# Kernel optimization log

Hardware: AMD Instinct MI355X
Metric: run time of the kernel (lower is better)

The kernel has to match this reference:

```python
import jax
import jax.numpy as jnp
import numpy as np
from jax.scipy.linalg import expm

H = 2048   # hidden_size
R = 1      # low-rank dimension
B = 2048   # batch of independent (h, x) pairs


def _glorot(key, shape):
    return jax.random.uniform(key, shape, minval=-1.0, maxval=1.0) * jnp.sqrt(2.0 / sum(shape))


def setup_inputs() -> dict:
    key = jax.random.key(0)
    k1, k2, k3, k4, k5, k6 = jax.random.split(key, 6)
    return {
        "h": jax.random.normal(k5, (B, H), dtype=jnp.float32),
        "x": jax.random.normal(k6, (B, H), dtype=jnp.float32),
        # a_diag ~ U(-1, 0) * init_scale (10.0): negative real diagonal
        "a_diag": jax.random.uniform(k1, (H,), minval=-1.0, maxval=0.0) * 10.0,
        "p_vec": _glorot(k2, (H, R)),
        "q_vec": _glorot(k3, (H, R)),
        "b_mat": _glorot(k4, (H, H)),
        "delta": jnp.array(0.1, dtype=jnp.float32),
    }


def reference(h, x, a_diag, p_vec, q_vec, b_mat, delta):
    # A = diag(a_diag) + P Q^T  (DPLR structure, materialized dense as in source)
    A = jnp.diag(a_diag) + p_vec @ q_vec.T                       # [H, H]
    # Discretized state matrix: exp(delta * A)
    expA = expm(delta * A)                                       # [H, H]
    # Discretized input matrix: A^{-1} (exp(delta A) - I) B  (pinv as in source)
    A_inv = jnp.linalg.pinv(A)                                   # [H, H]
    B_disc = A_inv @ (expA - jnp.eye(H, dtype=A.dtype)) @ b_mat  # [H, H]
    # Batched recurrence step: A h + B x  for each row of h, x
    return h @ expA.T + x @ B_disc.T                             # [B, H]
```

## Files before the change

kernel.cpp:

```cpp
#include <hip/hip_runtime.h>

#define MAXM 16
#define NL_CAP 256
#define THETA 0.02f
#define SMEM_BYTES 32768

typedef unsigned short u16;
typedef u16 u16x8 __attribute__((ext_vector_type(8)));
typedef u16 u16x4 __attribute__((ext_vector_type(4)));
typedef __bf16 bf16x8 __attribute__((ext_vector_type(8)));
typedef float f32x4 __attribute__((ext_vector_type(4)));


__device__ __forceinline__ u16 f2bf(float f) {
    unsigned u = __float_as_uint(f);
    return (u16)((u + 0x7fffu + ((u >> 16) & 1u)) >> 16);
}

__global__ __launch_bounds__(256)
void conv_k(const float* __restrict__ x, const float* __restrict__ b,
            u16* __restrict__ xb, u16* __restrict__ bb, long nx, long nb)
{
    long i = ((long)blockIdx.x * 256 + threadIdx.x) * 4;
    if (i < nx) {
        float4 v = *(const float4*)&x[i];
        u16x4 o = {f2bf(v.x), f2bf(v.y), f2bf(v.z), f2bf(v.w)};
        *(u16x4*)&xb[i] = o;
    }
    if (i < nb) {
        float4 v = *(const float4*)&b[i];
        u16x4 o = {f2bf(v.x), f2bf(v.y), f2bf(v.z), f2bf(v.w)};
        *(u16x4*)&bb[i] = o;
    }
}


__device__ __forceinline__ double frcp(double den) {
    double r = (double)__builtin_amdgcn_rcpf((float)den);
    return fma(r, fma(-den, r, 1.0), r);
}


__device__ __forceinline__ void gload_lds16(const void* g, void* l) {
    __builtin_amdgcn_global_load_lds(
        (const __attribute__((address_space(1))) unsigned int*)g,
        (__attribute__((address_space(3))) unsigned int*)l, 16, 0, 0);
}

__device__ __forceinline__ void gemm_tile(u16* Al, u16* Bl, int tid, int bx, int by,
                                          const u16* __restrict__ A,
                                          const u16* __restrict__ B,
                                          float* __restrict__ C,
                                          int Ndim, int Kstride, int Klen)
{
    const int bm = by * 128, bn = bx * 128;
    const int wv = tid >> 6, ln = tid & 63;
    const int wr = (wv >> 1) * 64, wc = (wv & 1) * 64;
    const int fr = ln & 15, fk = (ln >> 4) * 8;
    const int fk2 = fk ^ ((fr & 3) << 3);

    const int r0 = tid >> 2;
    const int c0 = ((tid & 3) ^ (r0 & 3)) * 8;
    const u16* Ap0 = A + (size_t)(bm + r0) * Kstride + c0;
    const u16* Ap1 = Ap0 + (size_t)64 * Kstride;
    const u16* Bp0 = B + (size_t)(bn + r0) * Kstride + c0;
    const u16* Bp1 = Bp0 + (size_t)64 * Kstride;

    f32x4 acc[4][4];
#pragma unroll
    for (int m = 0; m < 4; ++m)
#pragma unroll
        for (int n = 0; n < 4; ++n) acc[m][n] = (f32x4)0.f;

    {
        u16* a0 = Al + wv * 512;
        u16* a1 = Al + 2048 + wv * 512;
        u16* b0 = Bl + wv * 512;
        u16* b1 = Bl + 2048 + wv * 512;
        gload_lds16(Ap0, a0);
        gload_lds16(Ap1, a1);
        gload_lds16(Bp0, b0);
        gload_lds16(Bp1, b1);
    }

    int cur = 0;
    for (int kk = 0; kk < Klen; kk += 32) {
        const bool hasNext = (kk + 32 < Klen);
        if (hasNext) {
            const int nb = (cur ^ 1) * 4096;
            u16* a0 = Al + nb + wv * 512;
            u16* a1 = Al + nb + 2048 + wv * 512;
            u16* b0 = Bl + nb + wv * 512;
            u16* b1 = Bl + nb + 2048 + wv * 512;
            gload_lds16(Ap0 + kk + 32, a0);
            gload_lds16(Ap1 + kk + 32, a1);
            gload_lds16(Bp0 + kk + 32, b0);
            gload_lds16(Bp1 + kk + 32, b1);
            asm volatile("s_waitcnt vmcnt(4)" ::: "memory");
        } else {
            asm volatile("s_waitcnt vmcnt(0)" ::: "memory");
        }
        __builtin_amdgcn_sched_barrier(0);
        __builtin_amdgcn_s_barrier();

        const int cb = cur * 4096;
        u16x8 af[4], bf[4];
#pragma unroll
        for (int m = 0; m < 4; ++m)
            af[m] = *(const u16x8*)&Al[cb + (wr + m * 16 + fr) * 32 + fk2];
#pragma unroll
        for (int n = 0; n < 4; ++n)
            bf[n] = *(const u16x8*)&Bl[cb + (wc + n * 16 + fr) * 32 + fk2];
#pragma unroll
        for (int m = 0; m < 4; ++m)
#pragma unroll
            for (int n = 0; n < 4; ++n)
                acc[m][n] = __builtin_amdgcn_mfma_f32_16x16x32_bf16(
                    __builtin_bit_cast(bf16x8, af[m]),
                    __builtin_bit_cast(bf16x8, bf[n]), acc[m][n], 0, 0, 0);

        __builtin_amdgcn_sched_barrier(0);
        __builtin_amdgcn_s_barrier();
        cur ^= 1;
    }

    const int crow = (ln >> 4) * 4;
#pragma unroll
    for (int m = 0; m < 4; ++m)
#pragma unroll
        for (int n = 0; n < 4; ++n) {
            const size_t base = (size_t)(bm + wr + m * 16 + crow) * Ndim
                              + bn + wc + n * 16 + fr;
#pragma unroll
            for (int j = 0; j < 4; ++j)
                C[base + (size_t)j * Ndim] = acc[m][n][j];
        }
}

__global__ __launch_bounds__(256)
void bgemm_k(const u16* __restrict__ A, const u16* __restrict__ B,
             float* __restrict__ C, int Ndim, int Kdim)
{
    __shared__ __align__(16) unsigned char smem[SMEM_BYTES];
    gemm_tile((u16*)smem, (u16*)smem + 8192, threadIdx.x,
              blockIdx.x, blockIdx.y, A, B, C, Ndim, Kdim, Kdim);
}


__global__ __launch_bounds__(256)
void g_sgemm_k(const float* __restrict__ A, const float* __restrict__ B,
               float* __restrict__ C, int Mdim, int Ndim, int Kdim)
{
    __shared__ __align__(16) float As[16][132];
    __shared__ __align__(16) float Bs[16][68];
    const int tid = threadIdx.x;
    const int tx = tid & 15, ty = tid >> 4;
    const int bn = blockIdx.x * 64, bm = blockIdx.y * 128;
    const int lrA = tid >> 1, lcA = (tid & 1) << 3;
    const int lrB = tid >> 2, lcB = (tid & 3) << 2;
    const float* Aptr = A + (size_t)(bm + lrA) * Kdim + lcA;
    const float* Bptr = B + (size_t)(bn + lrB) * Kdim + lcB;
    float4 a0 = *(const float4*)(Aptr);
    float4 a1 = *(const float4*)(Aptr + 4);
    float4 b0 = *(const float4*)(Bptr);
    float acc[8][4];
#pragma unroll
    for (int i = 0; i < 8; ++i)
#pragma unroll
        for (int j = 0; j < 4; ++j) acc[i][j] = 0.f;
    for (int kk = 0; kk < Kdim; kk += 16) {
        __syncthreads();
        As[lcA + 0][lrA] = a0.x; As[lcA + 1][lrA] = a0.y;
        As[lcA + 2][lrA] = a0.z; As[lcA + 3][lrA] = a0.w;
        As[lcA + 4][lrA] = a1.x; As[lcA + 5][lrA] = a1.y;
        As[lcA + 6][lrA] = a1.z; As[lcA + 7][lrA] = a1.w;
        Bs[lcB + 0][lrB] = b0.x; Bs[lcB + 1][lrB] = b0.y;
        Bs[lcB + 2][lrB] = b0.z; Bs[lcB + 3][lrB] = b0.w;
        __syncthreads();
        if (kk + 16 < Kdim) {
            a0 = *(const float4*)(Aptr + kk + 16);
            a1 = *(const float4*)(Aptr + kk + 20);
            b0 = *(const float4*)(Bptr + kk + 16);
        }
#pragma unroll
        for (int k = 0; k < 16; ++k) {
            const float4 av0 = *(const float4*)&As[k][ty * 8];
            const float4 av1 = *(const float4*)&As[k][ty * 8 + 4];
            const float4 bv  = *(const float4*)&Bs[k][tx * 4];
            const float avf[8] = {av0.x, av0.y, av0.z, av0.w, av1.x, av1.y, av1.z, av1.w};
            const float bvf[4] = {bv.x, bv.y, bv.z, bv.w};
#pragma unroll
            for (int i = 0; i < 8; ++i)
#pragma unroll
                for (int j = 0; j < 4; ++j) acc[i][j] += avf[i] * bvf[j];
        }
    }
#pragma unroll
    for (int i = 0; i < 8; ++i) {
        const int r = bm + ty * 8 + i;
        float4 v = {acc[i][0], acc[i][1], acc[i][2], acc[i][3]};
        *(float4*)&C[(size_t)r * Ndim + bn + tx * 4] = v;
    }
}


__device__ __forceinline__ double wsum(double x) {
#pragma unroll
    for (int m = 32; m; m >>= 1) x += __shfl_xor(x, m, 64);
    return x;
}
__device__ __forceinline__ float wsumf(float x) {
#pragma unroll
    for (int m = 32; m; m >>= 1) x += __shfl_xor(x, m, 64);
    return x;
}

__device__ __forceinline__ int inert(double s11, double s12, double s22,
                                     double dc, double cS)
{
    double b00 = cS - s11, b01 = -1.0 - s12, b11 = -s22;
    double det = b00 * b11 - b01 * b01, tr = b00 + b11;
    int neg = (det > 0.0) ? ((tr < 0.0) ? 2 : 0) : 1;
    return (int)(dc + 0.5) + neg - 1;
}

__device__ __forceinline__ int lane_evalN32(float tf, double td, int n4,
    const float4* l0, const float4* l1, const float4* l2,
    const double* pc, bool poly, double cS,
    double& g11o, double& g12o, double& g22o)
{
    float s11 = 0.f, s12 = 0.f, s22 = 0.f, dc = 0.f;
#pragma unroll 4
    for (int i = 0; i < n4; ++i) {
        const float4 d4 = l0[i], x4 = l1[i], y4 = l2[i];
        const float dd[4] = {d4.x, d4.y, d4.z, d4.w};
        const float xx[4] = {x4.x, x4.y, x4.z, x4.w};
        const float yy[4] = {y4.x, y4.y, y4.z, y4.w};
#pragma unroll
        for (int e = 0; e < 4; ++e) {
            float den = dd[e] - tf;
            float mag = fmaxf(fabsf(den), 1e-30f);
            den = (den < 0.f) ? -mag : mag;
            const float inv = __builtin_amdgcn_rcpf(den);
            s11 = fmaf(xx[e] * xx[e], inv, s11);
            s12 = fmaf(xx[e] * yy[e], inv, s12);
            s22 = fmaf(yy[e] * yy[e], inv, s22);
            if (dd[e] < tf) dc += 1.f;
        }
    }
    double S11 = (double)s11, S12 = (double)s12, S22 = (double)s22;
    if (poly) {
        S11 += pc[0] + td * (pc[3] + td * (pc[6] + td * pc[9]));
        S12 += pc[1] + td * (pc[4] + td * (pc[7] + td * pc[10]));
        S22 += pc[2] + td * (pc[5] + td * (pc[8] + td * pc[11]));
    }
    g11o = S11; g12o = S12; g22o = S22;
    return inert(S11, S12, S22, (double)dc, cS);
}

__device__ void spec256(unsigned char* smem, int tid,
                        const float* __restrict__ av, const float* __restrict__ pv,
                        const float* __restrict__ qv, double* __restrict__ hdr,
                        float* __restrict__ V)
{
    __builtin_amdgcn_s_setprio(1);

    float* sd2 = (float*)smem;
    float* sw1 = sd2 + 2048;
    float* sw2 = sw1 + 2048;
    float* nl0 = sw2 + 2048;
    float* nl1 = nl0 + NL_CAP;
    float* nl2 = nl1 + NL_CAP;
    double* dsh = (double*)(nl2 + NL_CAP);
    int* ish = (int*)(dsh + 192);

    const int lane = tid & 63, wv = tid >> 6;
    const int j0 = tid * 8;

    float d2r[8], w1r[8], w2r[8];
    double cS = 0, n1 = 0, n2 = 0, mx = 0;
#pragma unroll
    for (int h = 0; h < 2; ++h) {
        float4 aa = *(const float4*)&av[j0 + h * 4];
        float4 pp = *(const float4*)&pv[j0 + h * 4];
        float4 qq = *(const float4*)&qv[j0 + h * 4];
        const float a4[4] = {aa.x, aa.y, aa.z, aa.w};
        const float p4[4] = {pp.x, pp.y, pp.z, pp.w};
        const float q4[4] = {qq.x, qq.y, qq.z, qq.w};
#pragma unroll
        for (int e = 0; e < 4; ++e) {
            const int ix = h * 4 + e;
            d2r[ix] = a4[e] * a4[e];
            w1r[ix] = a4[e] * p4[e];
            w2r[ix] = q4[e];
            sd2[j0 + ix] = d2r[ix]; sw1[j0 + ix] = w1r[ix]; sw2[j0 + ix] = w2r[ix];
            cS += (double)p4[e] * p4[e];
            n1 += (double)w1r[ix] * w1r[ix];
            n2 += (double)w2r[ix] * w2r[ix];
            mx = fmax(mx, (double)d2r[ix]);
        }
    }
    cS = wsum(cS); n1 = wsum(n1); n2 = wsum(n2);
#pragma unroll
    for (int m_ = 32; m_; m_ >>= 1) mx = fmax(mx, __shfl_xor(mx, m_, 64));
    __syncthreads();
    if (lane == 0) { dsh[wv] = cS; dsh[4 + wv] = n1; dsh[8 + wv] = n2; dsh[12 + wv] = mx; }
    __syncthreads();
    cS = 0; n1 = 0; n2 = 0; mx = 0;
    for (int w = 0; w < 4; ++w) {
        cS += dsh[w]; n1 += dsh[4 + w]; n2 += dsh[8 + w];
        mx = fmax(mx, dsh[12 + w]);
    }
    __syncthreads();

    const double pert = 2.0 * sqrt(n1 * n2) + cS * n2;
    double lo = fmax(0.0, mx - pert);
    double hi = mx + pert + 0.5;
    for (int r = 0; r < 3; ++r) {
        const double td = lo + (hi - lo) * (double)(wv + 1) / 5.0;
        const float tf = (float)td;
        float s11 = 0.f, s12 = 0.f, s22 = 0.f, dc = 0.f;
        for (int i4 = lane; i4 < 512; i4 += 64) {
            const float4 dd = ((const float4*)sd2)[i4];
            const float4 e1 = ((const float4*)sw1)[i4];
            const float4 e2 = ((const float4*)sw2)[i4];
            const float df[4] = {dd.x, dd.y, dd.z, dd.w};
            const float f1[4] = {e1.x, e1.y, e1.z, e1.w};
            const float f2[4] = {e2.x, e2.y, e2.z, e2.w};
#pragma unroll
            for (int e = 0; e < 4; ++e) {
                float den = df[e] - tf;
                float mag = fmaxf(fabsf(den), 1e-30f);
                den = (den < 0.f) ? -mag : mag;
                const float inv = __builtin_amdgcn_rcpf(den);
                s11 = fmaf(f1[e] * f1[e], inv, s11);
                s12 = fmaf(f1[e] * f2[e], inv, s12);
                s22 = fmaf(f2[e] * f2[e], inv, s22);
                if (df[e] < tf) dc += 1.f;
            }
        }
        s11 = wsumf(s11); s12 = wsumf(s12); s22 = wsumf(s22); dc = wsumf(dc);
        if (lane == 0)
            ish[wv] = inert((double)s11, (double)s12, (double)s22, (double)dc, cS);
        __syncthreads();
        double nlo = lo, nhi = hi;
        for (int i = 0; i < 4; ++i) {
            double ti = lo + (hi - lo) * (double)(i + 1) / 5.0;
            if (ish[i] >= 2048) { if (ti < nhi) nhi = ti; }
            else                { if (ti > nlo) nlo = ti; }
        }
        lo = nlo; hi = nhi;
        __syncthreads();
    }
    const double lmax = 0.5 * (lo + hi);
    const double rc = 10.0 * 2048.0 * 1.1920928955078125e-07;
    const double cut2 = rc * rc * lmax;

    int flags = 0, lc = 0;
#pragma unroll
    for (int e = 0; e < 8; ++e)
        if (d2r[e] < THETA) { flags |= (1 << e); ++lc; }
    int sc = lc;
#pragma unroll
    for (int off = 1; off < 64; off <<= 1) {
        int y = __shfl_up(sc, off, 64);
        if (lane >= off) sc += y;
    }
    const int wtot = __shfl(sc, 63, 64);
    const int excl = sc - lc;
    if (lane == 0) ish[4 + wv] = wtot;
    __syncthreads();
    int base = excl;
    for (int w = 0; w < wv; ++w) base += ish[4 + w];
    int cnt = 0;
    for (int w = 0; w < 4; ++w) cnt += ish[4 + w];
    {
        int pos = base;
#pragma unroll
        for (int e = 0; e < 8; ++e) {
            if (flags & (1 << e)) {
                if (pos < NL_CAP) { nl0[pos] = d2r[e]; nl1[pos] = w1r[e]; nl2[pos] = w2r[e]; }
                ++pos;
            }
        }
    }
    const int cntPad = (cnt + 7) & ~7;
    if (tid == 0) {
        for (int i = cnt; i < cntPad && i < NL_CAP; ++i) {
            nl0[i] = 1e30f; nl1[i] = 0.f; nl2[i] = 0.f;
        }
        ish[8] = cnt; ish[10] = cntPad >> 2;
    }

    float cff[12];
#pragma unroll
    for (int c = 0; c < 12; ++c) cff[c] = 0.f;
#pragma unroll
    for (int e = 0; e < 8; ++e) {
        if (d2r[e] >= THETA) {
            float id = __builtin_amdgcn_rcpf(d2r[e]);
            float b1 = w1r[e], b2 = w2r[e];
            float x11 = b1 * b1, x12 = b1 * b2, x22 = b2 * b2;
            float f = id;
            cff[0] += x11 * f; cff[1]  += x12 * f; cff[2]  += x22 * f; f *= id;
            cff[3] += x11 * f; cff[4]  += x12 * f; cff[5]  += x22 * f; f *= id;
            cff[6] += x11 * f; cff[7]  += x12 * f; cff[8]  += x22 * f; f *= id;
            cff[9] += x11 * f; cff[10] += x12 * f; cff[11] += x22 * f;
        }
    }
#pragma unroll
    for (int c = 0; c < 12; ++c) cff[c] = wsumf(cff[c]);
    if (lane == 0) {
        double* dw = &dsh[16 + wv * 12];
#pragma unroll
        for (int c = 0; c < 12; ++c) dw[c] = (double)cff[c];
    }
    __syncthreads();
    if (tid < 12) {
        double s = 0;
        for (int w = 0; w < 4; ++w) s += dsh[16 + w * 12 + tid];
        dsh[96 + tid] = s;
    }
    __syncthreads();

    cnt = ish[8];
    const bool nearOK = (cnt <= NL_CAP - 8);
    const float4* l0 = nearOK ? (const float4*)nl0 : (const float4*)sd2;
    const float4* l1 = nearOK ? (const float4*)nl1 : (const float4*)sw1;
    const float4* l2 = nearOK ? (const float4*)nl2 : (const float4*)sw2;
    const int n4 = nearOK ? ish[10] : 512;
    const bool poly = nearOK;
    const double* pcoef = &dsh[96];

    double zg1, zg2, zg3;
    if (wv == 0) {
        int N = lane_evalN32((float)cut2, cut2, n4, l0, l1, l2, pcoef, poly, cS,
                             zg1, zg2, zg3);
        if (lane == 0) ish[9] = N;
    }
    __syncthreads();
    int m = ish[9];
    if (m < 0) m = 0;
    if (m > MAXM) m = MAXM;

    for (int k = wv; k < m; k += 4) {
        double klo = 0.0, khi = cut2;
        for (int r = 0; r < 2; ++r) {
            const double w = khi - klo;
            const double td = klo + w * (double)(lane + 1) / 65.0;
            int N = lane_evalN32((float)td, td, n4, l0, l1, l2, pcoef, poly, cS,
                                 zg1, zg2, zg3);
            unsigned long long mask = __ballot(N >= k + 1);
            int j = (mask == 0ull) ? 64 : (__ffsll(mask) - 1);
            double nk = (j == 64) ? khi : (klo + w * (double)(j + 1) / 65.0);
            klo = klo + w * (double)j / 65.0;
            khi = nk;
        }
        const double lam = 0.5 * (klo + khi);
        double g11, g12, g22;
        lane_evalN32((float)lam, lam, n4, l0, l1, l2, pcoef, poly, cS, g11, g12, g22);
        const double m00 = 1.0 + g12, m01 = g11 + cS * g12;
        const double m10 = g22,       m11 = 1.0 + g12 + cS * g22;
        double y1, y2;
        if (m00 * m00 + m01 * m01 >= m10 * m10 + m11 * m11) { y1 = m01; y2 = -m00; }
        else                                                { y1 = m11; y2 = -m10; }
        double z1 = y2, z2 = y1 + cS * y2;
        const double zs = 1.0 / fmax(fmax(fabs(z1), fabs(z2)), 1e-300);
        if (lane == 0) {
            dsh[112 + 3 * k]     = lam;
            dsh[112 + 3 * k + 1] = z1 * zs;
            dsh[112 + 3 * k + 2] = z2 * zs;
        }
    }
    __syncthreads();

    for (int k = 0; k < m; ++k) {
        const double lam = dsh[112 + 3 * k];
        const float z1 = (float)dsh[112 + 3 * k + 1];
        const float z2 = (float)dsh[112 + 3 * k + 2];
        float vr[8];
        float pn = 0.f;
#pragma unroll
        for (int e = 0; e < 8; ++e) {
            const double dend = (double)d2r[e] - lam;
            float den = (float)dend;
            float mag = fmaxf(fabsf(den), 1e-12f);
            den = (den < 0.f) ? -mag : mag;
            const float vi = (w1r[e] * z1 + w2r[e] * z2) * __builtin_amdgcn_rcpf(den);
            pn = fmaf(vi, vi, pn);
            vr[e] = vi;
        }
        pn = wsumf(pn);
        if (lane == 0) dsh[160 + wv] = (double)pn;
        __syncthreads();
        double tot = 0;
        for (int w = 0; w < 4; ++w) tot += dsh[160 + w];
        const float inv = (float)(1.0 / sqrt(tot));
        float o0[8];
#pragma unroll
        for (int e = 0; e < 8; ++e) o0[e] = vr[e] * inv;
        *(float4*)&V[(size_t)k * 2048 + j0]     = *(float4*)&o0[0];
        *(float4*)&V[(size_t)k * 2048 + j0 + 4] = *(float4*)&o0[4];
        __syncthreads();
    }

    if (tid == 0) { hdr[0] = lmax; hdr[1] = cut2; hdr[2] = (double)m; hdr[3] = cS; }
    __builtin_amdgcn_s_setprio(0);
}


__global__ __launch_bounds__(256)
void fat_k(const u16* __restrict__ A, const u16* __restrict__ B,
           float* __restrict__ C0, float* __restrict__ C1,
           float* __restrict__ C2, float* __restrict__ C3,
           int Ndim, int Kdim, int ntiles, int nbx, int nsplit,
           const float* __restrict__ av, const float* __restrict__ pv,
           const float* __restrict__ qv, double* __restrict__ hdr,
           float* __restrict__ V)
{
    __shared__ __align__(16) unsigned char smem[SMEM_BYTES];
    const int bid = blockIdx.x;
    if (bid == 0) {
        spec256(smem, threadIdx.x, av, pv, qv, hdr, V);
        return;
    }
    if ((bid & 255) == 0) return;
    const int t = bid - 1 - (bid >> 8);
    if (t >= ntiles * nsplit) return;
    const int ks = t / ntiles;
    const int tt = t - ks * ntiles;
    const int Klen = Kdim / nsplit;
    float* Cdst = (ks == 0) ? C0 : (ks == 1) ? C1 : (ks == 2) ? C2 : C3;
    gemm_tile((u16*)smem, (u16*)smem + 8192, threadIdx.x,
              tt % nbx, tt / nbx,
              A + (size_t)ks * Klen, B + (size_t)ks * Klen,
              Cdst, Ndim, Kdim, Klen);
}


__global__ __launch_bounds__(256, 2)
void series_k(float* __restrict__ io, const float* __restrict__ p1,
              const float* __restrict__ p2, const float* __restrict__ p3,
              int nparts, const float* __restrict__ hm,
              const float* __restrict__ qv, const float* __restrict__ pv,
              const float* __restrict__ av, const float* __restrict__ delta,
              const float* __restrict__ V, const double* __restrict__ hdr,
              int useTrunc)
{
    const int lane = threadIdx.x & 63;
    const int row = blockIdx.x * 4 + (threadIdx.x >> 6);
    const float d = delta[0];
    const int m = useTrunc ? (int)hdr[2] : 0;

    float q[32], p[32], a[32], t[32], o[32];
    float* iorow = io + (size_t)row * 2048;
    const float* p1row = p1 + (size_t)row * 2048;
    const float* p2row = p2 + (size_t)row * 2048;
    const float* p3row = p3 + (size_t)row * 2048;
#pragma unroll
    for (int cc = 0; cc < 8; ++cc) {
        const int j = cc * 256 + lane * 4;
        *(float4*)&q[cc * 4] = *(const float4*)&qv[j];
        *(float4*)&p[cc * 4] = *(const float4*)&pv[j];
        *(float4*)&a[cc * 4] = *(const float4*)&av[j];
        float4 u0 = *(const float4*)&iorow[j];
        if (nparts >= 1) {
            const float4 u1 = *(const float4*)&p1row[j];
            u0.x += u1.x; u0.y += u1.y; u0.z += u1.z; u0.w += u1.w;
        }
        if (nparts >= 2) {
            const float4 u1 = *(const float4*)&p2row[j];
            u0.x += u1.x; u0.y += u1.y; u0.z += u1.z; u0.w += u1.w;
        }
        if (nparts >= 3) {
            const float4 u1 = *(const float4*)&p3row[j];
            u0.x += u1.x; u0.y += u1.y; u0.z += u1.z; u0.w += u1.w;
        }
        *(float4*)&t[cc * 4] = u0;
    }
#pragma unroll
    for (int e = 0; e < 32; ++e) o[e] = t[e];

    float cf = 1.f;
    for (int k = 1; k <= 13; ++k) {
        float s = 0.f;
#pragma unroll
        for (int e = 0; e < 32; ++e) s += t[e] * q[e];
#pragma unroll
        for (int msk = 32; msk; msk >>= 1) s += __shfl_xor(s, msk, 64);
        cf /= (float)(k + 1);
        const float ds = d * s;
#pragma unroll
        for (int e = 0; e < 32; ++e) { t[e] = d * a[e] * t[e] + ds * p[e]; o[e] += cf * t[e]; }
    }
#pragma unroll
    for (int e = 0; e < 32; ++e) o[e] *= d;

    for (int k = 0; k < m; ++k) {
        const float* vr = V + (size_t)k * 2048;
        float vk[32];
#pragma unroll
        for (int cc = 0; cc < 8; ++cc)
            *(float4*)&vk[cc * 4] = *(const float4*)&vr[cc * 256 + lane * 4];
        float s = 0.f;
#pragma unroll
        for (int e = 0; e < 32; ++e) s += o[e] * vk[e];
#pragma unroll
        for (int msk = 32; msk; msk >>= 1) s += __shfl_xor(s, msk, 64);
#pragma unroll
        for (int e = 0; e < 32; ++e) o[e] -= s * vk[e];
    }

    const float* hrow = hm + (size_t)row * 2048;
#pragma unroll
    for (int cc = 0; cc < 8; ++cc)
        *(float4*)&t[cc * 4] = *(const float4*)&hrow[cc * 256 + lane * 4];
#pragma unroll
    for (int e = 0; e < 32; ++e) o[e] += t[e];
    cf = 1.f;
    for (int k = 1; k <= 14; ++k) {
        float s = 0.f;
#pragma unroll
        for (int e = 0; e < 32; ++e) s += t[e] * q[e];
#pragma unroll
        for (int msk = 32; msk; msk >>= 1) s += __shfl_xor(s, msk, 64);
        cf /= (float)k;
        const float ds = d * s;
#pragma unroll
        for (int e = 0; e < 32; ++e) { t[e] = d * a[e] * t[e] + ds * p[e]; o[e] += cf * t[e]; }
    }
#pragma unroll
    for (int cc = 0; cc < 8; ++cc)
        *(float4*)&iorow[cc * 256 + lane * 4] = *(const float4*)&o[cc * 4];
}


extern "C" void kernel_launch(void* const* d_in, const int* in_sizes, int n_in,
                              void* d_out, int out_size, void* d_ws, size_t ws_size,
                              hipStream_t stream)
{
    const float* hmat  = (const float*)d_in[0];
    const float* xmat  = (const float*)d_in[1];
    const float* adiag = (const float*)d_in[2];
    const float* pvec  = (const float*)d_in[3];
    const float* qvec  = (const float*)d_in[4];
    const float* bmat  = (const float*)d_in[5];
    const float* delta = (const float*)d_in[6];
    float* out = (float*)d_out;

    const int H  = in_sizes[2];
    const int Bb = in_sizes[0] / H;
    const size_t SZ = (size_t)Bb * H;
    const size_t HH = (size_t)H * H;

    double* hdr = (double*)d_ws;
    float* V = (float*)(hdr + 8);
    u16* xb = (u16*)(V + (size_t)MAXM * H);
    u16* bb = xb + SZ;
    float* C1 = (float*)(bb + HH);
    float* C2 = C1 + SZ;
    float* C3 = C2 + SZ;

    const size_t needSpec = 64 + (size_t)MAXM * H * sizeof(float);
    const size_t needFull = needSpec + (SZ + HH) * sizeof(u16);
    const size_t needS2   = needFull + SZ * sizeof(float);
    const size_t needS4   = needFull + 3 * SZ * sizeof(float);
    const bool doTrunc = (H == 2048) && (ws_size >= needSpec);
    const bool doBf16  = (ws_size >= needFull) && (H % 128 == 0) && (Bb % 128 == 0);
    int nsplit = 1;
    if (doBf16 && doTrunc) {
        if (ws_size >= needS4) nsplit = 4;
        else if (ws_size >= needS2) nsplit = 2;
    }
    const int nparts = nsplit - 1;

    dim3 blk256(256);
    const int nbx = H / 128;
    const int ntiles = nbx * (Bb / 128);

    if (doBf16) {
        const long nmax = (long)(SZ > HH ? SZ : HH);
        const int cg = (int)((nmax / 4 + 255) / 256);
        conv_k<<<cg, blk256, 0, stream>>>(xmat, bmat, xb, bb, (long)SZ, (long)HH);
        if (doTrunc) {
            const int NT = ntiles * nsplit;
            const int grid = 1 + NT + (NT + 254) / 255;
            fat_k<<<grid, blk256, 0, stream>>>(
                xb, bb, out, C1, C2, C3, H, H, ntiles, nbx, nsplit,
                adiag, pvec, qvec, hdr, V);
        } else {
            dim3 gg(nbx, Bb / 128);
            bgemm_k<<<gg, blk256, 0, stream>>>(xb, bb, out, H, H);
        }
    } else {
        if (doTrunc)
            fat_k<<<1, blk256, 0, stream>>>(nullptr, nullptr, out, nullptr,
                                            nullptr, nullptr, H, H, 0, 1, 1,
                                            adiag, pvec, qvec, hdr, V);
        dim3 gg(H / 64, Bb / 128);
        g_sgemm_k<<<gg, blk256, 0, stream>>>(xmat, bmat, out, Bb, H, H);
    }

    series_k<<<Bb / 4, blk256, 0, stream>>>(out,
                                            nparts >= 1 ? C1 : out,
                                            nparts >= 2 ? C2 : out,
                                            nparts >= 3 ? C3 : out,
                                            nparts,
                                            hmat, qvec, pvec, adiag, delta,
                                            V, hdr, doTrunc ? 1 : 0);
}
```

Measured before the change: 79.82 us.

## Replace 4-way split-K with balanced stream-K partition over 510 GEMM blocks

```diff
diff --git a/kernel.cpp b/kernel.cpp
--- a/kernel.cpp
+++ b/kernel.cpp
@@ -137,15 +137,6 @@
         }
 }
 
-__global__ __launch_bounds__(256)
-void bgemm_k(const u16* __restrict__ A, const u16* __restrict__ B,
-             float* __restrict__ C, int Ndim, int Kdim)
-{
-    __shared__ __align__(16) unsigned char smem[SMEM_BYTES];
-    gemm_tile((u16*)smem, (u16*)smem + 8192, threadIdx.x,
-              blockIdx.x, blockIdx.y, A, B, C, Ndim, Kdim, Kdim);
-}
-
 
 __global__ __launch_bounds__(256)
 void g_sgemm_k(const float* __restrict__ A, const float* __restrict__ B,
@@ -512,36 +503,50 @@
 __global__ __launch_bounds__(256)
 void fat_k(const u16* __restrict__ A, const u16* __restrict__ B,
            float* __restrict__ C0, float* __restrict__ C1,
-           float* __restrict__ C2, float* __restrict__ C3,
-           int Ndim, int Kdim, int ntiles, int nbx, int nsplit,
+           float* __restrict__ C2,
+           int Ndim, int Kdim, int nbx, int balanced, int ntiles,
            const float* __restrict__ av, const float* __restrict__ pv,
            const float* __restrict__ qv, double* __restrict__ hdr,
            float* __restrict__ V)
 {
     __shared__ __align__(16) unsigned char smem[SMEM_BYTES];
+    u16* Al = (u16*)smem;
+    u16* Bl = (u16*)smem + 8192;
     const int bid = blockIdx.x;
     if (bid == 0) {
         spec256(smem, threadIdx.x, av, pv, qv, hdr, V);
         return;
     }
     if ((bid & 255) == 0) return;
-    const int t = bid - 1 - (bid >> 8);
-    if (t >= ntiles * nsplit) return;
-    const int ks = t / ntiles;
-    const int tt = t - ks * ntiles;
-    const int Klen = Kdim / nsplit;
-    float* Cdst = (ks == 0) ? C0 : (ks == 1) ? C1 : (ks == 2) ? C2 : C3;
-    gemm_tile((u16*)smem, (u16*)smem + 8192, threadIdx.x,
-              tt % nbx, tt / nbx,
-              A + (size_t)ks * Klen, B + (size_t)ks * Klen,
-              Cdst, Ndim, Kdim, Klen);
+    const int i = bid - 1 - (bid >> 8);
+    if (balanced) {
+        if (i >= 510) return;
+        const long S = (i < 64) ? 1056L * i : 67584L + 1024L * (i - 64);
+        const int L = (i < 64) ? 1056 : 1024;
+        const int t0 = (int)(S >> 11);
+        const int k0 = (int)(S & 2047);
+        const int len1 = (L < 2048 - k0) ? L : (2048 - k0);
+        float* Cs = (k0 == 0) ? C0 : ((k0 < 1024) ? C1 : C2);
+        gemm_tile(Al, Bl, threadIdx.x, t0 % nbx, t0 / nbx,
+                  A + k0, B + k0, Cs, Ndim, Kdim, len1);
+        if (len1 < L) {
+            __syncthreads();
+            const int t1 = t0 + 1;
+            gemm_tile(Al, Bl, threadIdx.x, t1 % nbx, t1 / nbx,
+                      A, B, C0, Ndim, Kdim, L - len1);
+        }
+    } else {
+        if (i >= ntiles) return;
+        gemm_tile(Al, Bl, threadIdx.x, i % nbx, i / nbx,
+                  A, B, C0, Ndim, Kdim, Kdim);
+    }
 }
 
 
 __global__ __launch_bounds__(256, 2)
 void series_k(float* __restrict__ io, const float* __restrict__ p1,
-              const float* __restrict__ p2, const float* __restrict__ p3,
-              int nparts, const float* __restrict__ hm,
+              const float* __restrict__ p2, int nparts,
+              const float* __restrict__ hm,
               const float* __restrict__ qv, const float* __restrict__ pv,
               const float* __restrict__ av, const float* __restrict__ delta,
               const float* __restrict__ V, const double* __restrict__ hdr,
@@ -556,7 +561,6 @@
     float* iorow = io + (size_t)row * 2048;
     const float* p1row = p1 + (size_t)row * 2048;
     const float* p2row = p2 + (size_t)row * 2048;
-    const float* p3row = p3 + (size_t)row * 2048;
 #pragma unroll
     for (int cc = 0; cc < 8; ++cc) {
         const int j = cc * 256 + lane * 4;
@@ -572,10 +576,6 @@
             const float4 u1 = *(const float4*)&p2row[j];
             u0.x += u1.x; u0.y += u1.y; u0.z += u1.z; u0.w += u1.w;
         }
-        if (nparts >= 3) {
-            const float4 u1 = *(const float4*)&p3row[j];
-            u0.x += u1.x; u0.y += u1.y; u0.z += u1.z; u0.w += u1.w;
-        }
         *(float4*)&t[cc * 4] = u0;
     }
 #pragma unroll
@@ -659,20 +659,13 @@
     u16* bb = xb + SZ;
     float* C1 = (float*)(bb + HH);
     float* C2 = C1 + SZ;
-    float* C3 = C2 + SZ;
 
     const size_t needSpec = 64 + (size_t)MAXM * H * sizeof(float);
     const size_t needFull = needSpec + (SZ + HH) * sizeof(u16);
-    const size_t needS2   = needFull + SZ * sizeof(float);
-    const size_t needS4   = needFull + 3 * SZ * sizeof(float);
+    const size_t needBal  = needFull + 2 * SZ * sizeof(float);
     const bool doTrunc = (H == 2048) && (ws_size >= needSpec);
     const bool doBf16  = (ws_size >= needFull) && (H % 128 == 0) && (Bb % 128 == 0);
-    int nsplit = 1;
-    if (doBf16 && doTrunc) {
-        if (ws_size >= needS4) nsplit = 4;
-        else if (ws_size >= needS2) nsplit = 2;
-    }
-    const int nparts = nsplit - 1;
+    const bool doBal   = doBf16 && doTrunc && (Bb == 2048) && (ws_size >= needBal);
 
     dim3 blk256(256);
     const int nbx = H / 128;
@@ -683,29 +676,36 @@
         const int cg = (int)((nmax / 4 + 255) / 256);
         conv_k<<<cg, blk256, 0, stream>>>(xmat, bmat, xb, bb, (long)SZ, (long)HH);
         if (doTrunc) {
-            const int NT = ntiles * nsplit;
-            const int grid = 1 + NT + (NT + 254) / 255;
+            if (doBal) {
+                hipMemsetAsync(C1, 0, 2 * SZ * sizeof(float), stream);
+                fat_k<<<513, blk256, 0, stream>>>(
+                    xb, bb, out, C1, C2, H, H, nbx, 1, ntiles,
+                    adiag, pvec, qvec, hdr, V);
+            } else {
+                const int grid = 1 + ntiles + (ntiles + 254) / 255;
+                fat_k<<<grid, blk256, 0, stream>>>(
+                    xb, bb, out, C1, C2, H, H, nbx, 0, ntiles,
+                    adiag, pvec, qvec, hdr, V);
+            }
+        } else {
+            const int grid = 1 + ntiles + (ntiles + 254) / 255;
             fat_k<<<grid, blk256, 0, stream>>>(
-                xb, bb, out, C1, C2, C3, H, H, ntiles, nbx, nsplit,
-                adiag, pvec, qvec, hdr, V);
-        } else {
-            dim3 gg(nbx, Bb / 128);
-            bgemm_k<<<gg, blk256, 0, stream>>>(xb, bb, out, H, H);
+                xb, bb, out, C1, C2, H, H, nbx, 0, ntiles,
+                nullptr, nullptr, nullptr, hdr, V);
         }
     } else {
         if (doTrunc)
-            fat_k<<<1, blk256, 0, stream>>>(nullptr, nullptr, out, nullptr,
-                                            nullptr, nullptr, H, H, 0, 1, 1,
+            fat_k<<<1, blk256, 0, stream>>>(nullptr, nullptr, out, nullptr, nullptr,
+                                            H, H, 1, 0, 0,
                                             adiag, pvec, qvec, hdr, V);
         dim3 gg(H / 64, Bb / 128);
         g_sgemm_k<<<gg, blk256, 0, stream>>>(xmat, bmat, out, Bb, H, H);
     }
 
     series_k<<<Bb / 4, blk256, 0, stream>>>(out,
-                                            nparts >= 1 ? C1 : out,
-                                            nparts >= 2 ? C2 : out,
-                                            nparts >= 3 ? C3 : out,
-                                            nparts,
+                                            doBal ? C1 : out,
+                                            doBal ? C2 : out,
+                                            doBal ? 2 : 0,
                                             hmat, qvec, pvec, adiag, delta,
                                             V, hdr, doTrunc ? 1 : 0);
 }
```

Result: slower. 82.68 us (+3.6%).
